# Kernel optimization log

Measured on AMD Instinct MI355X. Metric: run time of the kernel, lower is better.

The kernel has to match this reference:

```python
import jax, jax.numpy as jnp
import numpy as np
from functools import partial

D_MODEL = 1024
D_HIDDEN = 4096
N_BLOCKS = 4
D_VOCAB = 32000
BATCH = 2
SEQ = 2048
LN_EPS = 1e-5
LRELU_SLOPE = 0.01  # torch nn.LeakyReLU default


def setup_inputs() -> dict:
    key = jax.random.key(0)
    ks = jax.random.split(key, 16)
    d, h, L, v = D_MODEL, D_HIDDEN, N_BLOCKS, D_VOCAB
    scale = d ** 0.5
    inp = {
        "tokens": jax.random.randint(ks[0], (BATCH, SEQ), 0, v, dtype=jnp.int64)
                  if jax.config.jax_enable_x64 else
                  jax.random.randint(ks[0], (BATCH, SEQ), 0, v, dtype=jnp.int32),
        "emb": jax.random.normal(ks[1], (v, d), jnp.float32) * 0.02,
        # per-block stacked params (leading axis = layer) for lax.scan
        "qk": jax.random.normal(ks[2], (L, d, d), jnp.float32) / scale,
        "ov": jax.random.normal(ks[3], (L, d, d), jnp.float32) / scale,
        "w_up": jax.random.normal(ks[4], (L, d, h), jnp.float32) / scale,
        "b_up": jnp.zeros((L, h), jnp.float32),
        "w_hid": jax.random.normal(ks[5], (L, h, h), jnp.float32) / (h ** 0.5),
        "b_hid": jnp.zeros((L, h), jnp.float32),
        "w_down": jax.random.normal(ks[6], (L, h, d), jnp.float32) / (h ** 0.5),
        "b_down": jnp.zeros((L, d), jnp.float32),
        "ln1_g": jnp.ones((L, d), jnp.float32),
        "ln1_b": jnp.zeros((L, d), jnp.float32),
        "ln2_g": jnp.ones((L, d), jnp.float32),
        "ln2_b": jnp.zeros((L, d), jnp.float32),
    }
    return inp


def _layer_norm(x, g, b):
    mu = jnp.mean(x, axis=-1, keepdims=True)
    var = jnp.mean(jnp.square(x - mu), axis=-1, keepdims=True)
    return (x - mu) * jax.lax.rsqrt(var + LN_EPS) * g + b


def _forward(tokens, emb, qk, ov, w_up, b_up, w_hid, b_hid, w_down, b_down,
             ln1_g, ln1_b, ln2_g, ln2_b):
    x = emb[tokens]                                   # [B, S, D]
    seq = tokens.shape[1]
    scale = jnp.asarray(D_MODEL ** 0.5, x.dtype)
    causal = jnp.tril(jnp.ones((seq, seq), bool))     # True = keep

    def block(x, p):
        (qk, ov, w_up, b_up, w_hid, b_hid, w_down, b_down,
         g1, b1, g2, b2) = p
        h = _layer_norm(x, g1, b1)
        # attention: (h @ qk @ h^T) / sqrt(d), causal mask, softmax, @ h @ ov
        scores = jnp.einsum('bsd,de,bte->bst', h, qk, h) / scale
        scores = jnp.where(causal, scores, -jnp.inf)
        attn = jax.nn.softmax(scores, axis=-1)
        x = x + jnp.einsum('bst,btd,de->bse', attn, h, ov)
        # MLP with LeakyReLU after every layer (incl. output)
        m = _layer_norm(x, g2, b2)
        m = jax.nn.leaky_relu(m @ w_up + b_up, LRELU_SLOPE)
        m = jax.nn.leaky_relu(m @ w_hid + b_hid, LRELU_SLOPE)
        m = jax.nn.leaky_relu(m @ w_down + b_down, LRELU_SLOPE)
        return x + m, None

    params = (qk, ov, w_up, b_up, w_hid, b_hid, w_down, b_down,
              ln1_g, ln1_b, ln2_g, ln2_b)
    x, _ = jax.lax.scan(block, x, params)
    return x @ emb.T                                  # [B, S, V] logits


@jax.jit
def reference(tokens, emb, qk, ov, w_up, b_up, w_hid, b_hid, w_down, b_down,
              ln1_g, ln1_b, ln2_g, ln2_b):
    return _forward(tokens, emb, qk, ov, w_up, b_up, w_hid, b_hid,
                    w_down, b_down, ln1_g, ln1_b, ln2_g, ln2_b)
```

## Files before the change

kernel.cpp:

```cpp
#include <hip/hip_runtime.h>

#define BS   4096
#define SEQL 2048
#define DM   1024
#define DH   4096
#define NV   32000

using u16 = unsigned short;

typedef __attribute__((ext_vector_type(8))) short bf16x8;
typedef __attribute__((ext_vector_type(4))) float f32x4;

__device__ __forceinline__ u16 f2b(float f) {
  union { float f; unsigned u; } c; c.f = f;
  unsigned u = c.u;
  u = (u + 0x7FFFu + ((u >> 16) & 1u)) >> 16;
  return (u16)u;
}

__device__ __forceinline__ void gld16(const u16* g, u16* l) {
  __builtin_amdgcn_global_load_lds(
      (__attribute__((address_space(1))) void*)(void*)const_cast<u16*>(g),
      (__attribute__((address_space(3))) void*)l, 16, 0, 0);
}

__global__ __launch_bounds__(256) void k_embed(const int* __restrict__ tok,
                                               const float* __restrict__ emb,
                                               float* __restrict__ x) {
  const long row = blockIdx.x;
  const long e = tok[row];
  ((float4*)(x + row * DM))[threadIdx.x] = ((const float4*)(emb + e * DM))[threadIdx.x];
}

__global__ __launch_bounds__(256) void k_cvt(const float* __restrict__ in,
                                             u16* __restrict__ out, int n4) {
  int i = blockIdx.x * 256 + threadIdx.x;
  if (i < n4) {
    float4 v = ((const float4*)in)[i];
    ushort4 o;
    o.x = f2b(v.x); o.y = f2b(v.y); o.z = f2b(v.z); o.w = f2b(v.w);
    ((ushort4*)out)[i] = o;
  }
}

__global__ __launch_bounds__(256) void k_ln(const float* __restrict__ x,
                                            const float* __restrict__ g,
                                            const float* __restrict__ b,
                                            u16* __restrict__ out) {
  const long row = blockIdx.x;
  const int t = threadIdx.x;
  float4 v = ((const float4*)(x + row * DM))[t];
  float s  = v.x + v.y + v.z + v.w;
  float q2 = v.x*v.x + v.y*v.y + v.z*v.z + v.w*v.w;
#pragma unroll
  for (int o = 1; o < 64; o <<= 1) { s += __shfl_xor(s, o); q2 += __shfl_xor(q2, o); }
  __shared__ float rs_[4], rq_[4];
  const int lane = t & 63, wid = t >> 6;
  if (lane == 0) { rs_[wid] = s; rq_[wid] = q2; }
  __syncthreads();
  s  = rs_[0] + rs_[1] + rs_[2] + rs_[3];
  q2 = rq_[0] + rq_[1] + rq_[2] + rq_[3];
  const float mu   = s * (1.f / 1024.f);
  const float var  = q2 * (1.f / 1024.f) - mu * mu;
  const float rstd = rsqrtf(var + 1e-5f);
  float4 gg = ((const float4*)g)[t];
  float4 bb = ((const float4*)b)[t];
  ushort4 o;
  o.x = f2b((v.x - mu) * rstd * gg.x + bb.x);
  o.y = f2b((v.y - mu) * rstd * gg.y + bb.y);
  o.z = f2b((v.z - mu) * rstd * gg.z + bb.z);
  o.w = f2b((v.w - mu) * rstd * gg.w + bb.w);
  ((ushort4*)(out + row * DM))[t] = o;
}

__device__ __forceinline__ u16 to_b16(float v) { return f2b(v); }
__device__ __forceinline__ u16 to_b16(u16 v)   { return v; }

template <typename T>
__global__ __launch_bounds__(256) void k_transpose(const T* __restrict__ in,
                                                   u16* __restrict__ out,
                                                   int R, int C, long inz, long outz) {
  __shared__ u16 tile[32][33];
  const T* ip = in + (long)blockIdx.z * inz;
  u16* op = out + (long)blockIdx.z * outz;
  const int tx = threadIdx.x & 31, ty = threadIdx.x >> 5;
  const long c0 = (long)blockIdx.x * 32, r0 = (long)blockIdx.y * 32;
#pragma unroll
  for (int i = 0; i < 4; ++i)
    tile[ty + i * 8][tx] = to_b16(ip[(r0 + ty + i * 8) * C + c0 + tx]);
  __syncthreads();
#pragma unroll
  for (int i = 0; i < 4; ++i)
    op[(c0 + ty + i * 8) * R + r0 + tx] = tile[tx][ty + i * 8];
}

__global__ __launch_bounds__(256) void k_softmax(const float* __restrict__ sc,
                                                 u16* __restrict__ at) {
  const int r = blockIdx.x;
  const long z = blockIdx.y;
  const int t = threadIdx.x;
  const float* row = sc + (z * SEQL + r) * SEQL;
  u16* orow = at + (z * SEQL + r) * SEQL;
  float vals[8];
  float mx = -3.4e38f;
#pragma unroll
  for (int i = 0; i < 8; ++i) {
    int c = i * 256 + t;
    float v = (c <= r) ? row[c] : -3.4e38f;
    vals[i] = v;
    mx = fmaxf(mx, v);
  }
#pragma unroll
  for (int o = 1; o < 64; o <<= 1) mx = fmaxf(mx, __shfl_xor(mx, o));
  __shared__ float rm[4], rsum[4];
  const int lane = t & 63, wid = t >> 6;
  if (lane == 0) rm[wid] = mx;
  __syncthreads();
  mx = fmaxf(fmaxf(rm[0], rm[1]), fmaxf(rm[2], rm[3]));
  float sum = 0.f;
#pragma unroll
  for (int i = 0; i < 8; ++i) {
    int c = i * 256 + t;
    float e = (c <= r) ? __expf(vals[i] - mx) : 0.f;
    vals[i] = e;
    sum += e;
  }
#pragma unroll
  for (int o = 1; o < 64; o <<= 1) sum += __shfl_xor(sum, o);
  if (lane == 0) rsum[wid] = sum;
  __syncthreads();
  sum = rsum[0] + rsum[1] + rsum[2] + rsum[3];
  const float inv = 1.f / sum;
#pragma unroll
  for (int i = 0; i < 8; ++i) orow[i * 256 + t] = f2b(vals[i] * inv);
}

template <int EPI, bool BIAS, bool LRELU, int CAUSAL, bool SWZ>
__global__ __launch_bounds__(256, 2) void k_gemm_bt(
    const u16* __restrict__ A, const u16* __restrict__ B, void* __restrict__ C,
    const float* __restrict__ bias, int K, int N,
    long sAz, long sBz, long sCz, float scale) {
  __shared__ u16 lA[128 * 32];
  __shared__ u16 lB[128 * 32];
  const int t = threadIdx.x;
  const long z = blockIdx.z;
  int bx = blockIdx.x, by = blockIdx.y;
  if (SWZ) {
    int id = bx + gridDim.x * by;
    int cpx = (gridDim.x * gridDim.y) >> 3;
    int s = (id & 7) * cpx + (id >> 3);
    bx = s % gridDim.x;
    by = s / gridDim.x;
  }
  const long row0 = (long)bx * 128;
  const long col0 = (long)by * 128;
  if (CAUSAL == 1 && col0 > row0 + 127) return;
  const int Klim = (CAUSAL == 2) ? min(K, (int)row0 + 128) : K;
  const u16* Ab = A + z * sAz;
  const u16* Bb = B + z * sBz;

  const int rr = t >> 2;
  const int c8 = (t & 3) * 8;
  const u16* gA0 = Ab + (row0 + rr) * K + c8;
  const u16* gA1 = Ab + (row0 + 64 + rr) * K + c8;
  const u16* gB0 = Bb + (col0 + rr) * K + c8;
  const u16* gB1 = Bb + (col0 + 64 + rr) * K + c8;
  u16* sA0 = &lA[rr * 32 + c8];
  u16* sA1 = &lA[(64 + rr) * 32 + c8];
  u16* sB0 = &lB[rr * 32 + c8];
  u16* sB1 = &lB[(64 + rr) * 32 + c8];

  const int lane = t & 63;
  const int w = t >> 6;
  const int wr = (w >> 1) * 64, wc = (w & 1) * 64;
  const int fr = lane & 15;
  const int fk = (lane >> 4) * 8;

  f32x4 acc[4][4] = {};

  for (int k0 = 0; k0 < Klim; k0 += 32) {
    gld16(gA0 + k0, sA0);
    gld16(gA1 + k0, sA1);
    gld16(gB0 + k0, sB0);
    gld16(gB1 + k0, sB1);
    __syncthreads();
    bf16x8 av[4], bv[4];
#pragma unroll
    for (int m = 0; m < 4; ++m) av[m] = *(const bf16x8*)&lA[(wr + m * 16 + fr) * 32 + fk];
#pragma unroll
    for (int n = 0; n < 4; ++n) bv[n] = *(const bf16x8*)&lB[(wc + n * 16 + fr) * 32 + fk];
#pragma unroll
    for (int m = 0; m < 4; ++m)
#pragma unroll
      for (int n = 0; n < 4; ++n)
        acc[m][n] = __builtin_amdgcn_mfma_f32_16x16x32_bf16(av[m], bv[n], acc[m][n], 0, 0, 0);
    __syncthreads();
  }

  const int er = (lane >> 4) * 4;
  const int ec = lane & 15;
#pragma unroll
  for (int m = 0; m < 4; ++m) {
#pragma unroll
    for (int n = 0; n < 4; ++n) {
#pragma unroll
      for (int j = 0; j < 4; ++j) {
        long r = row0 + wr + m * 16 + er + j;
        long c = col0 + wc + n * 16 + ec;
        float v = acc[m][n][j] * scale;
        if (BIAS)  v += bias[c];
        if (LRELU) v = v > 0.f ? v : 0.01f * v;
        if (EPI == 0)      ((float*)C)[z * sCz + r * (long)N + c] = v;
        else if (EPI == 1) ((u16*)C)[z * sCz + r * (long)N + c] = f2b(v);
        else               ((float*)C)[z * sCz + r * (long)N + c] += v;
      }
    }
  }
}

extern "C" void kernel_launch(void* const* d_in, const int* in_sizes, int n_in,
                              void* d_out, int out_size, void* d_ws, size_t ws_size,
                              hipStream_t stream) {
  const int*   tokens = (const int*)d_in[0];
  const float* emb    = (const float*)d_in[1];
  const float* qk     = (const float*)d_in[2];
  const float* ov     = (const float*)d_in[3];
  const float* wup    = (const float*)d_in[4];
  const float* bup    = (const float*)d_in[5];
  const float* whid   = (const float*)d_in[6];
  const float* bhid   = (const float*)d_in[7];
  const float* wdown  = (const float*)d_in[8];
  const float* bdown  = (const float*)d_in[9];
  const float* g1     = (const float*)d_in[10];
  const float* b1     = (const float*)d_in[11];
  const float* g2     = (const float*)d_in[12];
  const float* b2     = (const float*)d_in[13];

  char* Ob = (char*)d_out;
  float* scores = (float*)(Ob + 0);
  u16*   attn   = (u16*)(Ob + 33554432);
  u16*   m1     = (u16*)(Ob + 50331648);
  u16*   m2     = (u16*)(Ob + 83886080);
  u16*   qkT    = (u16*)(Ob + 117440512);
  u16*   ovT    = (u16*)(Ob + 125829120);
  u16*   upT    = (u16*)(Ob + 134217728);
  u16*   hidT   = (u16*)(Ob + 167772160);
  u16*   downT  = (u16*)(Ob + 301989888);
  float* xres   = (float*)(Ob + 335544320);
  u16*   h      = (u16*)(Ob + 352321536);
  u16*   hT     = (u16*)(Ob + 360710144);
  u16*   q      = (u16*)(Ob + 369098752);
  u16*   attnV  = (u16*)(Ob + 377487360);

  u16* embB = (u16*)d_ws;
  u16* xB   = (u16*)((char*)d_ws + 65536000);

  k_embed<<<dim3(BS), 256, 0, stream>>>(tokens, emb, xres);
  k_cvt<<<dim3(32000), 256, 0, stream>>>(emb, embB, 8192000);

  k_transpose<float><<<dim3(32, 32, 4),   256, 0, stream>>>(qk,    qkT,   1024, 1024, 1048576,  1048576);
  k_transpose<float><<<dim3(32, 32, 4),   256, 0, stream>>>(ov,    ovT,   1024, 1024, 1048576,  1048576);
  k_transpose<float><<<dim3(128, 32, 4),  256, 0, stream>>>(wup,   upT,   1024, 4096, 4194304,  4194304);
  k_transpose<float><<<dim3(128, 128, 4), 256, 0, stream>>>(whid,  hidT,  4096, 4096, 16777216, 16777216);
  k_transpose<float><<<dim3(32, 128, 4),  256, 0, stream>>>(wdown, downT, 4096, 1024, 4194304,  4194304);

  for (int l = 0; l < 4; ++l) {
    k_ln<<<dim3(BS), 256, 0, stream>>>(xres, g1 + l * 1024, b1 + l * 1024, h);
    k_transpose<u16><<<dim3(32, 64, 2), 256, 0, stream>>>(h, hT, 2048, 1024, 2048L * 1024, 1024L * 2048);
    k_gemm_bt<1, false, false, 0, false><<<dim3(32, 8, 1), 256, 0, stream>>>(
        h, qkT + (long)l * 1048576, q, nullptr, 1024, 1024, 0, 0, 0, 0.03125f);
    k_gemm_bt<0, false, false, 1, false><<<dim3(16, 16, 2), 256, 0, stream>>>(
        q, h, scores, nullptr, 1024, 2048, 2048L * 1024, 2048L * 1024, 2048L * 2048, 1.f);
    k_softmax<<<dim3(2048, 2), 256, 0, stream>>>(scores, attn);
    k_gemm_bt<1, false, false, 2, false><<<dim3(16, 8, 2), 256, 0, stream>>>(
        attn, hT, attnV, nullptr, 2048, 1024, 2048L * 2048, 1024L * 2048, 2048L * 1024, 1.f);
    k_gemm_bt<2, false, false, 0, false><<<dim3(32, 8, 1), 256, 0, stream>>>(
        attnV, ovT + (long)l * 1048576, xres, nullptr, 1024, 1024, 0, 0, 0, 1.f);

    k_ln<<<dim3(BS), 256, 0, stream>>>(xres, g2 + l * 1024, b2 + l * 1024, h);
    k_gemm_bt<1, true, true, 0, false><<<dim3(32, 32, 1), 256, 0, stream>>>(
        h, upT + (long)l * 4194304, m1, bup + l * 4096, 1024, 4096, 0, 0, 0, 1.f);
    k_gemm_bt<1, true, true, 0, false><<<dim3(32, 32, 1), 256, 0, stream>>>(
        m1, hidT + (long)l * 16777216, m2, bhid + l * 4096, 4096, 4096, 0, 0, 0, 1.f);
    k_gemm_bt<2, true, true, 0, false><<<dim3(32, 8, 1), 256, 0, stream>>>(
        m2, downT + (long)l * 4194304, xres, bdown + l * 1024, 4096, 1024, 0, 0, 0, 1.f);
  }

  k_cvt<<<dim3(4096), 256, 0, stream>>>(xres, xB, 1048576);
  k_gemm_bt<0, false, false, 0, true><<<dim3(32, 250, 1), 256, 0, stream>>>(
      xB, embB, (float*)d_out, nullptr, 1024, 32000, 0, 0, 0, 1.f);
}
```

Before: 2.379 ms.

## Add 256x256 double-buffered GEMM kernel for MLP and vocab projections

Introduces a new 512-thread GEMM kernel with 256x256 output tiles, K-step of 64, double-buffered LDS staging via global_load_lds, an XOR swizzle against LDS bank conflicts, and MFMA priority hints. It replaces the 128x128 kernel for the up, hidden and final vocab projections to raise arithmetic intensity and overlap loads with compute. The block-swizzle option is removed from the old kernel. The larger tiles use 128 KB of LDS and many accumulator registers per block, which may limit occupancy, and launch fewer blocks per grid.

```diff
diff --git a/kernel.cpp b/kernel.cpp
--- a/kernel.cpp
+++ b/kernel.cpp
@@ -135,7 +135,7 @@
   for (int i = 0; i < 8; ++i) orow[i * 256 + t] = f2b(vals[i] * inv);
 }
 
-template <int EPI, bool BIAS, bool LRELU, int CAUSAL, bool SWZ>
+template <int EPI, bool BIAS, bool LRELU, int CAUSAL>
 __global__ __launch_bounds__(256, 2) void k_gemm_bt(
     const u16* __restrict__ A, const u16* __restrict__ B, void* __restrict__ C,
     const float* __restrict__ bias, int K, int N,
@@ -144,16 +144,8 @@
   __shared__ u16 lB[128 * 32];
   const int t = threadIdx.x;
   const long z = blockIdx.z;
-  int bx = blockIdx.x, by = blockIdx.y;
-  if (SWZ) {
-    int id = bx + gridDim.x * by;
-    int cpx = (gridDim.x * gridDim.y) >> 3;
-    int s = (id & 7) * cpx + (id >> 3);
-    bx = s % gridDim.x;
-    by = s / gridDim.x;
-  }
-  const long row0 = (long)bx * 128;
-  const long col0 = (long)by * 128;
+  const long row0 = (long)blockIdx.x * 128;
+  const long col0 = (long)blockIdx.y * 128;
   if (CAUSAL == 1 && col0 > row0 + 127) return;
   const int Klim = (CAUSAL == 2) ? min(K, (int)row0 + 128) : K;
   const u16* Ab = A + z * sAz;
@@ -213,6 +205,108 @@
         if (EPI == 0)      ((float*)C)[z * sCz + r * (long)N + c] = v;
         else if (EPI == 1) ((u16*)C)[z * sCz + r * (long)N + c] = f2b(v);
         else               ((float*)C)[z * sCz + r * (long)N + c] += v;
+      }
+    }
+  }
+}
+
+template <int EPI, bool BIAS, bool LRELU>
+__global__ __launch_bounds__(512, 2) void k_gemm256(
+    const u16* __restrict__ A, const u16* __restrict__ B, void* __restrict__ C,
+    const float* __restrict__ bias, int K, int N, float scale) {
+  __shared__ u16 S[2][2][16384];
+  const int t = threadIdx.x;
+  const int lane = t & 63;
+  const int w = t >> 6;
+  const int wr = w >> 2;
+  const int wc = w & 3;
+  const long row0 = (long)blockIdx.x * 256;
+  const long col0 = (long)blockIdx.y * 256;
+  const int nt = K >> 6;
+
+  const u16* pA[4];
+  const u16* pB[4];
+  int ldsoff[4];
+#pragma unroll
+  for (int i = 0; i < 4; ++i) {
+    int d = t * 16 + i * 8192;
+    int dx = d ^ (((d >> 9) & 1) << 5);
+    int srow = dx >> 7;
+    int scol = (dx & 127) >> 1;
+    ldsoff[i] = d >> 1;
+    pA[i] = A + (row0 + srow) * (long)K + scol;
+    pB[i] = B + (col0 + srow) * (long)K + scol;
+  }
+
+  const int fr = lane & 15;
+  const int fky = lane >> 4;
+  const int flip = (fr & 4) ? 32 : 0;
+  const int aoff = (((wr * 128 + fr) * 128) + fky * 16) ^ flip;
+  const int boff = (((wc * 64 + fr) * 128) + fky * 16) ^ flip;
+
+  f32x4 acc[8][4] = {};
+
+  auto STAGE = [&](int b) {
+    u16* SA = &S[b][0][0];
+    u16* SB = &S[b][1][0];
+#pragma unroll
+    for (int i = 0; i < 4; ++i) gld16(pA[i], SA + ldsoff[i]);
+#pragma unroll
+    for (int i = 0; i < 4; ++i) gld16(pB[i], SB + ldsoff[i]);
+#pragma unroll
+    for (int i = 0; i < 4; ++i) { pA[i] += 64; pB[i] += 64; }
+  };
+
+  auto COMPUTE = [&](int b) {
+    const char* Ab = (const char*)&S[b][0][0] + aoff;
+    const char* Bb = (const char*)&S[b][1][0] + boff;
+    bf16x8 bv[8];
+#pragma unroll
+    for (int n = 0; n < 4; ++n)
+#pragma unroll
+      for (int kk = 0; kk < 2; ++kk)
+        bv[n * 2 + kk] = *(const bf16x8*)(Bb + n * 2048 + kk * 64);
+    __builtin_amdgcn_s_setprio(1);
+#pragma unroll
+    for (int m = 0; m < 8; ++m) {
+      bf16x8 a0 = *(const bf16x8*)(Ab + m * 2048);
+      bf16x8 a1 = *(const bf16x8*)(Ab + m * 2048 + 64);
+#pragma unroll
+      for (int n = 0; n < 4; ++n)
+        acc[m][n] = __builtin_amdgcn_mfma_f32_16x16x32_bf16(a0, bv[n * 2], acc[m][n], 0, 0, 0);
+#pragma unroll
+      for (int n = 0; n < 4; ++n)
+        acc[m][n] = __builtin_amdgcn_mfma_f32_16x16x32_bf16(a1, bv[n * 2 + 1], acc[m][n], 0, 0, 0);
+    }
+    __builtin_amdgcn_s_setprio(0);
+  };
+
+  STAGE(0);
+  __syncthreads();
+  int cur = 0;
+  for (int tt = 0; tt < nt; ++tt) {
+    if (tt + 1 < nt) STAGE(cur ^ 1);
+    COMPUTE(cur);
+    __syncthreads();
+    cur ^= 1;
+  }
+
+  const int er = (lane >> 4) * 4;
+  const int ec = lane & 15;
+#pragma unroll
+  for (int m = 0; m < 8; ++m) {
+#pragma unroll
+    for (int n = 0; n < 4; ++n) {
+#pragma unroll
+      for (int j = 0; j < 4; ++j) {
+        long r = row0 + wr * 128 + m * 16 + er + j;
+        long c = col0 + wc * 64 + n * 16 + ec;
+        float v = acc[m][n][j] * scale;
+        if (BIAS)  v += bias[c];
+        if (LRELU) v = v > 0.f ? v : 0.01f * v;
+        if (EPI == 0)      ((float*)C)[r * (long)N + c] = v;
+        else if (EPI == 1) ((u16*)C)[r * (long)N + c] = f2b(v);
+        else               ((float*)C)[r * (long)N + c] += v;
       }
     }
   }
@@ -267,26 +361,26 @@
   for (int l = 0; l < 4; ++l) {
     k_ln<<<dim3(BS), 256, 0, stream>>>(xres, g1 + l * 1024, b1 + l * 1024, h);
     k_transpose<u16><<<dim3(32, 64, 2), 256, 0, stream>>>(h, hT, 2048, 1024, 2048L * 1024, 1024L * 2048);
-    k_gemm_bt<1, false, false, 0, false><<<dim3(32, 8, 1), 256, 0, stream>>>(
+    k_gemm_bt<1, false, false, 0><<<dim3(32, 8, 1), 256, 0, stream>>>(
         h, qkT + (long)l * 1048576, q, nullptr, 1024, 1024, 0, 0, 0, 0.03125f);
-    k_gemm_bt<0, false, false, 1, false><<<dim3(16, 16, 2), 256, 0, stream>>>(
+    k_gemm_bt<0, false, false, 1><<<dim3(16, 16, 2), 256, 0, stream>>>(
         q, h, scores, nullptr, 1024, 2048, 2048L * 1024, 2048L * 1024, 2048L * 2048, 1.f);
     k_softmax<<<dim3(2048, 2), 256, 0, stream>>>(scores, attn);
-    k_gemm_bt<1, false, false, 2, false><<<dim3(16, 8, 2), 256, 0, stream>>>(
+    k_gemm_bt<1, false, false, 2><<<dim3(16, 8, 2), 256, 0, stream>>>(
         attn, hT, attnV, nullptr, 2048, 1024, 2048L * 2048, 1024L * 2048, 2048L * 1024, 1.f);
-    k_gemm_bt<2, false, false, 0, false><<<dim3(32, 8, 1), 256, 0, stream>>>(
+    k_gemm_bt<2, false, false, 0><<<dim3(32, 8, 1), 256, 0, stream>>>(
         attnV, ovT + (long)l * 1048576, xres, nullptr, 1024, 1024, 0, 0, 0, 1.f);
 
     k_ln<<<dim3(BS), 256, 0, stream>>>(xres, g2 + l * 1024, b2 + l * 1024, h);
-    k_gemm_bt<1, true, true, 0, false><<<dim3(32, 32, 1), 256, 0, stream>>>(
-        h, upT + (long)l * 4194304, m1, bup + l * 4096, 1024, 4096, 0, 0, 0, 1.f);
-    k_gemm_bt<1, true, true, 0, false><<<dim3(32, 32, 1), 256, 0, stream>>>(
-        m1, hidT + (long)l * 16777216, m2, bhid + l * 4096, 4096, 4096, 0, 0, 0, 1.f);
-    k_gemm_bt<2, true, true, 0, false><<<dim3(32, 8, 1), 256, 0, stream>>>(
+    k_gemm256<1, true, true><<<dim3(16, 16), 512, 0, stream>>>(
+        h, upT + (long)l * 4194304, m1, bup + l * 4096, 1024, 4096, 1.f);
+    k_gemm256<1, true, true><<<dim3(16, 16), 512, 0, stream>>>(
+        m1, hidT + (long)l * 16777216, m2, bhid + l * 4096, 4096, 4096, 1.f);
+    k_gemm_bt<2, true, true, 0><<<dim3(32, 8, 1), 256, 0, stream>>>(
         m2, downT + (long)l * 4194304, xres, bdown + l * 1024, 4096, 1024, 0, 0, 0, 1.f);
   }
 
   k_cvt<<<dim3(4096), 256, 0, stream>>>(xres, xB, 1048576);
-  k_gemm_bt<0, false, false, 0, true><<<dim3(32, 250, 1), 256, 0, stream>>>(
-      xB, embB, (float*)d_out, nullptr, 1024, 32000, 0, 0, 0, 1.f);
-}
+  k_gemm256<0, false, false><<<dim3(16, 125), 512, 0, stream>>>(
+      xB, embB, (float*)d_out, nullptr, 1024, 32000, 1.f);
+}
```

New measurement: 2.140 ms. 10.1% less time.
